# Kernel optimization log

Measured on AMD Instinct MI355X. Metric: run time of the kernel, lower is better.

The kernel has to match this reference:

```python
import jax, jax.numpy as jnp
import numpy as np

# Qwen3 MoE sparse block reference.
# E experts, top-k routing with softmax probs, normalized top-k weights,
# gated-SiLU expert MLPs (gate/up H->I, down I->H), weighted scatter-combine.
E, K, H, I = 8, 2, 2048, 768
B, S = 2, 2048


def setup_inputs() -> dict:
    key = jax.random.key(0)
    k0, k1, k2, k3, k4 = jax.random.split(key, 5)
    hidden_states = jax.random.normal(k0, (B, S, H), jnp.float32)
    w_router = jax.random.normal(k1, (H, E), jnp.float32) * (1.0 / np.sqrt(H))
    wi0 = jax.random.normal(k2, (E, H, I), jnp.float32) * 0.02  # gate proj
    wi1 = jax.random.normal(k3, (E, H, I), jnp.float32) * 0.02  # up proj
    wo = jax.random.normal(k4, (E, I, H), jnp.float32) * 0.02   # down proj
    return {"hidden_states": hidden_states, "w_router": w_router,
            "wi0": wi0, "wi1": wi1, "wo": wo}


def _moe(hidden_states, w_router, wi0, wi1, wo):
    b, s, h = hidden_states.shape
    x = hidden_states.reshape(-1, h)                       # [T, H]
    router_logits = x @ w_router                           # [T, E]
    probs = jax.nn.softmax(router_logits.astype(jnp.float32), axis=-1)
    top_w, top_i = jax.lax.top_k(probs, K)                 # [T, K]
    # norm_topk_prob = True
    top_w = top_w / jnp.sum(top_w, axis=-1, keepdims=True)
    top_w = top_w.astype(x.dtype)
    # per-(expert, token) combine weight; zero for unrouted pairs -> same math
    # as the original gather/MLP/scatter-add over selected tokens.
    onehot = jax.nn.one_hot(top_i, E, dtype=x.dtype)       # [T, K, E]
    comb = jnp.einsum('tk,tke->et', top_w, onehot)         # [E, T]
    g = jax.nn.silu(jnp.einsum('th,ehi->eti', x, wi0))     # [E, T, I]
    u = jnp.einsum('th,ehi->eti', x, wi1)                  # [E, T, I]
    y = jnp.einsum('eti,eih->eth', g * u, wo)              # [E, T, H]
    out = jnp.einsum('et,eth->th', comb, y)                # [T, H]
    return out.reshape(b, s, h), router_logits


def reference(hidden_states, w_router, wi0, wi1, wo):
    return _moe(hidden_states, w_router, wi0, wi1, wo)
```

## Files before the change

### kernel.cpp

```cpp
#include <hip/hip_runtime.h>

#define T_TOK 4096
#define H_DIM 2048
#define I_DIM 768
#define E_NUM 8

typedef __attribute__((ext_vector_type(8))) short bf16x8;
typedef __attribute__((ext_vector_type(4))) float f32x4;

__device__ __forceinline__ unsigned short f2bf(float f) {
  union { float f; unsigned int u; } c; c.f = f;
  unsigned int r = c.u + 0x7fffu + ((c.u >> 16) & 1u);
  return (unsigned short)(r >> 16);
}

__device__ __forceinline__ void gl_lds16(const unsigned short* g, unsigned short* l) {
  __builtin_amdgcn_global_load_lds(
      (const __attribute__((address_space(1))) unsigned int*)g,
      (__attribute__((address_space(3))) unsigned int*)l, 16, 0, 0);
}

__global__ __launch_bounds__(256) void transpose_cast_kernel(
    const float* __restrict__ src, unsigned short* __restrict__ dst,
    int K, int N)
{
  const int e = blockIdx.z;
  const int kb = blockIdx.y * 64, nb = blockIdx.x * 64;
  src += (size_t)e * K * N + (size_t)kb * N + nb;
  dst += (size_t)e * N * K + (size_t)nb * K + kb;
  __shared__ float tile[64][65];
  const int tid = threadIdx.x;
  const int lr = tid >> 4, lc = (tid & 15) * 4;
#pragma unroll
  for (int it = 0; it < 4; ++it) {
    float4 v = *(const float4*)(src + (size_t)(lr + it * 16) * N + lc);
    tile[lr + it * 16][lc]     = v.x;
    tile[lr + it * 16][lc + 1] = v.y;
    tile[lr + it * 16][lc + 2] = v.z;
    tile[lr + it * 16][lc + 3] = v.w;
  }
  __syncthreads();
  const int wn = tid >> 2, wk = (tid & 3) * 16;
  union { uint4 u[2]; unsigned short h[16]; } o;
#pragma unroll
  for (int j = 0; j < 16; ++j) o.h[j] = f2bf(tile[wk + j][wn]);
  *(uint4*)(dst + (size_t)wn * K + wk)     = o.u[0];
  *(uint4*)(dst + (size_t)wn * K + wk + 8) = o.u[1];
}

#define RTOK 8
__global__ __launch_bounds__(256) void router_kernel(
    const float* __restrict__ x,
    const float* __restrict__ wr,
    unsigned short* __restrict__ xbf,
    float* __restrict__ logits_out,
    int* __restrict__ counts,
    int* __restrict__ entries,
    float* __restrict__ entry_w)
{
  const int tid = threadIdx.x;
  const int w = tid >> 6, lane = tid & 63;
  const int t0 = blockIdx.x * RTOK;
  const int hb = w * 512 + lane * 8;

  float wreg[8][8];
#pragma unroll
  for (int r = 0; r < 8; ++r) {
    *(float4*)&wreg[r][0] = *(const float4*)(wr + (size_t)(hb + r) * E_NUM);
    *(float4*)&wreg[r][4] = *(const float4*)(wr + (size_t)(hb + r) * E_NUM + 4);
  }

  __shared__ float red[RTOK][4][E_NUM];
  __shared__ float lg[RTOK][E_NUM];
  __shared__ int   ch_i[RTOK][2];
  __shared__ float ch_w[RTOK][2];

  for (int tt = 0; tt < RTOK; ++tt) {
    const int t = t0 + tt;
    float xv[8];
    *(float4*)&xv[0] = *(const float4*)(x + (size_t)t * H_DIM + hb);
    *(float4*)&xv[4] = *(const float4*)(x + (size_t)t * H_DIM + hb + 4);
    union { uint4 u; unsigned short h[8]; } o;
#pragma unroll
    for (int j = 0; j < 8; ++j) o.h[j] = f2bf(xv[j]);
    *(uint4*)(xbf + (size_t)t * H_DIM + hb) = o.u;

    float acc[E_NUM];
#pragma unroll
    for (int e = 0; e < E_NUM; ++e) acc[e] = 0.f;
#pragma unroll
    for (int r = 0; r < 8; ++r)
#pragma unroll
      for (int e = 0; e < E_NUM; ++e) acc[e] = fmaf(xv[r], wreg[r][e], acc[e]);
#pragma unroll
    for (int off = 32; off > 0; off >>= 1)
#pragma unroll
      for (int e = 0; e < E_NUM; ++e) acc[e] += __shfl_down(acc[e], off);
    if (lane == 0)
#pragma unroll
      for (int e = 0; e < E_NUM; ++e) red[tt][w][e] = acc[e];
  }
  __syncthreads();

  if (tid < RTOK * E_NUM) {
    const int tt = tid >> 3, e = tid & 7;
    float l = red[tt][0][e] + red[tt][1][e] + red[tt][2][e] + red[tt][3][e];
    lg[tt][e] = l;
    logits_out[(size_t)(t0 + tt) * E_NUM + e] = l;
  }
  __syncthreads();

  if (tid < RTOK) {
    const int tt = tid;
    float m1 = lg[tt][0]; int i1 = 0;
#pragma unroll
    for (int e = 1; e < E_NUM; ++e) if (lg[tt][e] > m1) { m1 = lg[tt][e]; i1 = e; }
    float m2 = -3.4e38f; int i2 = -1;
#pragma unroll
    for (int e = 0; e < E_NUM; ++e) if (e != i1 && lg[tt][e] > m2) { m2 = lg[tt][e]; i2 = e; }
    float w1 = 1.f / (1.f + __expf(m2 - m1));
    ch_i[tt][0] = i1; ch_i[tt][1] = i2;
    ch_w[tt][0] = w1; ch_w[tt][1] = 1.f - w1;
  }
  __syncthreads();

  if (tid < E_NUM) {
    const int e = tid;
    int cnt = 0;
#pragma unroll
    for (int tt = 0; tt < RTOK; ++tt) {
      if (ch_i[tt][0] == e) ++cnt;
      if (ch_i[tt][1] == e) ++cnt;
    }
    if (cnt > 0) {
      int base = atomicAdd(&counts[e], cnt);
      int pos = 0;
#pragma unroll
      for (int tt = 0; tt < RTOK; ++tt) {
#pragma unroll
        for (int k = 0; k < 2; ++k) {
          if (ch_i[tt][k] == e) {
            entries[e * T_TOK + base + pos] = (t0 + tt) * 2 + k;
            entry_w[e * T_TOK + base + pos] = ch_w[tt][k];
            ++pos;
          }
        }
      }
    }
  }
}

#define FRAG(arr, row, cb) \
  (*(const bf16x8*)(&(arr)[((row) << 6) + ((((cb)) ^ ((row) & 7)) << 3)]))

#define MAX_MB 72

__global__ __launch_bounds__(256) void moe_up_kernel(
    const unsigned short* __restrict__ xbf,
    const unsigned short* __restrict__ wgt,
    const unsigned short* __restrict__ wut,
    const int* __restrict__ counts,
    const int* __restrict__ entries,
    unsigned short* __restrict__ act)
{
  const int bid = blockIdx.x;
  const int nb = bid % (I_DIM / 64);
  const int mbl = bid / (I_DIM / 64);
  int e = -1, m0 = 0, cnt = 0, cum = 0;
#pragma unroll
  for (int ee = 0; ee < E_NUM; ++ee) {
    int c = counts[ee];
    int nmb = (c + 127) >> 7;
    if (e < 0 && mbl < cum + nmb) { e = ee; m0 = (mbl - cum) << 7; cnt = c; }
    cum += nmb;
  }
  if (e < 0) return;
  const int n0 = nb * 64;
  const int tid = threadIdx.x;

  __shared__ __align__(16) unsigned short As[128 * 64];
  __shared__ __align__(16) unsigned short Bg[64 * 64];
  __shared__ __align__(16) unsigned short Bu[64 * 64];
  __shared__ int rowp[128];

  if (tid < 128) rowp[tid] = (m0 + tid < cnt) ? entries[e * T_TOK + m0 + tid] : -1;
  __syncthreads();

  const int w = tid >> 6, lane = tid & 63;
  const int lrow = lane >> 3, lchunk = lane & 7;
  const int jj = lchunk ^ lrow;

  const unsigned short* wg_e = wgt + (size_t)e * I_DIM * H_DIM + (size_t)n0 * H_DIM;
  const unsigned short* wu_e = wut + (size_t)e * I_DIM * H_DIM + (size_t)n0 * H_DIM;
  const unsigned short* gA[4];
  unsigned short* lA[4];
#pragma unroll
  for (int t4 = 0; t4 < 4; ++t4) {
    int r = (t4 * 4 + w) * 8 + lrow;
    int p = rowp[r];
    int tok = (p >= 0) ? (p >> 1) : 0;
    gA[t4] = xbf + (size_t)tok * H_DIM + jj * 8;
    lA[t4] = As + (t4 * 4 + w) * 512;
  }
  const unsigned short* gG[2]; const unsigned short* gU[2]; unsigned short* lG[2]; unsigned short* lU[2];
#pragma unroll
  for (int t2 = 0; t2 < 2; ++t2) {
    int r = (t2 * 4 + w) * 8 + lrow;
    gG[t2] = wg_e + (size_t)r * H_DIM + jj * 8;
    gU[t2] = wu_e + (size_t)r * H_DIM + jj * 8;
    lG[t2] = Bg + (t2 * 4 + w) * 512;
    lU[t2] = Bu + (t2 * 4 + w) * 512;
  }

  f32x4 accg[4][2], accu[4][2];
#pragma unroll
  for (int i = 0; i < 4; ++i)
#pragma unroll
    for (int j = 0; j < 2; ++j) {
      accg[i][j] = (f32x4){0.f, 0.f, 0.f, 0.f};
      accu[i][j] = (f32x4){0.f, 0.f, 0.f, 0.f};
    }

  const int msub = (w >> 1) * 64, nsub = (w & 1) * 32;
  const int fm = lane & 15, fq = lane >> 4;

  for (int kt = 0; kt < H_DIM; kt += 64) {
#pragma unroll
    for (int t4 = 0; t4 < 4; ++t4) gl_lds16(gA[t4] + kt, lA[t4]);
#pragma unroll
    for (int t2 = 0; t2 < 2; ++t2) {
      gl_lds16(gG[t2] + kt, lG[t2]);
      gl_lds16(gU[t2] + kt, lU[t2]);
    }
    __syncthreads();
#pragma unroll
    for (int ks = 0; ks < 64; ks += 32) {
      const int cb = (ks >> 3) + fq;
      bf16x8 a[4], bg[2], bu[2];
#pragma unroll
      for (int mi = 0; mi < 4; ++mi)
        a[mi] = FRAG(As, msub + mi * 16 + fm, cb);
#pragma unroll
      for (int ni = 0; ni < 2; ++ni) {
        bg[ni] = FRAG(Bg, nsub + ni * 16 + fm, cb);
        bu[ni] = FRAG(Bu, nsub + ni * 16 + fm, cb);
      }
#pragma unroll
      for (int mi = 0; mi < 4; ++mi)
#pragma unroll
        for (int ni = 0; ni < 2; ++ni) {
          accg[mi][ni] = __builtin_amdgcn_mfma_f32_16x16x32_bf16(a[mi], bg[ni], accg[mi][ni], 0, 0, 0);
          accu[mi][ni] = __builtin_amdgcn_mfma_f32_16x16x32_bf16(a[mi], bu[ni], accu[mi][ni], 0, 0, 0);
        }
    }
    __syncthreads();
  }
#pragma unroll
  for (int mi = 0; mi < 4; ++mi) {
#pragma unroll
    for (int r = 0; r < 4; ++r) {
      int ml = msub + mi * 16 + fq * 4 + r;
      int p = rowp[ml];
      if (p < 0) continue;
      size_t base = (size_t)p * I_DIM + n0 + nsub + fm;
#pragma unroll
      for (int ni = 0; ni < 2; ++ni) {
        float g = accg[mi][ni][r];
        float u = accu[mi][ni][r];
        float h = g / (1.f + __expf(-g)) * u;
        act[base + ni * 16] = f2bf(h);
      }
    }
  }
}

__global__ __launch_bounds__(256) void moe_down_kernel(
    const unsigned short* __restrict__ act,
    const unsigned short* __restrict__ wot,
    const int* __restrict__ counts,
    const int* __restrict__ entries,
    const float* __restrict__ entry_w,
    float* __restrict__ out)
{
  const int bid = blockIdx.x;
  const int nb = bid % (H_DIM / 128);
  const int mbl = bid / (H_DIM / 128);
  int e = -1, m0 = 0, cnt = 0, cum = 0;
#pragma unroll
  for (int ee = 0; ee < E_NUM; ++ee) {
    int c = counts[ee];
    int nmb = (c + 127) >> 7;
    if (e < 0 && mbl < cum + nmb) { e = ee; m0 = (mbl - cum) << 7; cnt = c; }
    cum += nmb;
  }
  if (e < 0) return;
  const int n0 = nb * 128;
  const int tid = threadIdx.x;

  __shared__ __align__(16) unsigned short As[128 * 64];
  __shared__ __align__(16) unsigned short Bt[128 * 64];
  __shared__ int rowp[128];
  __shared__ float roww[128];

  if (tid < 128) {
    int idx = m0 + tid;
    rowp[tid] = (idx < cnt) ? entries[e * T_TOK + idx] : -1;
    roww[tid] = (idx < cnt) ? entry_w[e * T_TOK + idx] : 0.f;
  }
  __syncthreads();

  const int w = tid >> 6, lane = tid & 63;
  const int lrow = lane >> 3, lchunk = lane & 7;
  const int jj = lchunk ^ lrow;

  const unsigned short* wo_e = wot + (size_t)e * H_DIM * I_DIM + (size_t)n0 * I_DIM;
  const unsigned short* gA[4]; unsigned short* lA[4];
  const unsigned short* gB[4]; unsigned short* lB[4];
#pragma unroll
  for (int t4 = 0; t4 < 4; ++t4) {
    int r = (t4 * 4 + w) * 8 + lrow;
    int p = rowp[r];
    int pr = (p >= 0) ? p : 0;
    gA[t4] = act + (size_t)pr * I_DIM + jj * 8;
    lA[t4] = As + (t4 * 4 + w) * 512;
    gB[t4] = wo_e + (size_t)r * I_DIM + jj * 8;
    lB[t4] = Bt + (t4 * 4 + w) * 512;
  }

  f32x4 acc[4][4];
#pragma unroll
  for (int i = 0; i < 4; ++i)
#pragma unroll
    for (int j = 0; j < 4; ++j) acc[i][j] = (f32x4){0.f, 0.f, 0.f, 0.f};

  const int msub = (w >> 1) * 64, nsub = (w & 1) * 64;
  const int fm = lane & 15, fq = lane >> 4;

  for (int kt = 0; kt < I_DIM; kt += 64) {
#pragma unroll
    for (int t4 = 0; t4 < 4; ++t4) {
      gl_lds16(gA[t4] + kt, lA[t4]);
      gl_lds16(gB[t4] + kt, lB[t4]);
    }
    __syncthreads();
#pragma unroll
    for (int ks = 0; ks < 64; ks += 32) {
      const int cb = (ks >> 3) + fq;
      bf16x8 a[4], b[4];
#pragma unroll
      for (int mi = 0; mi < 4; ++mi)
        a[mi] = FRAG(As, msub + mi * 16 + fm, cb);
#pragma unroll
      for (int ni = 0; ni < 4; ++ni)
        b[ni] = FRAG(Bt, nsub + ni * 16 + fm, cb);
#pragma unroll
      for (int mi = 0; mi < 4; ++mi)
#pragma unroll
        for (int ni = 0; ni < 4; ++ni)
          acc[mi][ni] = __builtin_amdgcn_mfma_f32_16x16x32_bf16(a[mi], b[ni], acc[mi][ni], 0, 0, 0);
    }
    __syncthreads();
  }
#pragma unroll
  for (int mi = 0; mi < 4; ++mi) {
#pragma unroll
    for (int r = 0; r < 4; ++r) {
      int ml = msub + mi * 16 + fq * 4 + r;
      int p = rowp[ml];
      if (p < 0) continue;
      float wt = roww[ml];
      float* dst = out + (size_t)(p >> 1) * H_DIM + n0 + nsub + fm;
#pragma unroll
      for (int ni = 0; ni < 4; ++ni)
        atomicAdd(dst + ni * 16, acc[mi][ni][r] * wt);
    }
  }
}

extern "C" void kernel_launch(void* const* d_in, const int* in_sizes, int n_in,
                              void* d_out, int out_size, void* d_ws, size_t ws_size,
                              hipStream_t stream) {
  const float* x   = (const float*)d_in[0];
  const float* wr  = (const float*)d_in[1];
  const float* wi0 = (const float*)d_in[2];
  const float* wi1 = (const float*)d_in[3];
  const float* wo  = (const float*)d_in[4];
  float* out = (float*)d_out;
  float* logits_out = out + (size_t)T_TOK * H_DIM;

  char* w = (char*)d_ws;
  int* counts    = (int*)w;
  int* entries   = (int*)(w + 64);
  float* entry_w = (float*)(w + 64 + (size_t)E_NUM * T_TOK * 4);
  size_t off = 64 + 2 * (size_t)E_NUM * T_TOK * 4;
  unsigned short* xbf = (unsigned short*)(w + off); off += (size_t)T_TOK * H_DIM * 2;
  unsigned short* wgt = (unsigned short*)(w + off); off += (size_t)E_NUM * H_DIM * I_DIM * 2;
  unsigned short* wut = (unsigned short*)(w + off); off += (size_t)E_NUM * H_DIM * I_DIM * 2;
  unsigned short* wot = (unsigned short*)(w + off); off += (size_t)E_NUM * H_DIM * I_DIM * 2;
  unsigned short* act = (unsigned short*)(w + off);

  hipMemsetAsync(d_out, 0, (size_t)T_TOK * H_DIM * sizeof(float), stream);
  hipMemsetAsync(counts, 0, 64, stream);
  transpose_cast_kernel<<<dim3(I_DIM / 64, H_DIM / 64, E_NUM), 256, 0, stream>>>(
      wi0, wgt, H_DIM, I_DIM);
  transpose_cast_kernel<<<dim3(I_DIM / 64, H_DIM / 64, E_NUM), 256, 0, stream>>>(
      wi1, wut, H_DIM, I_DIM);
  transpose_cast_kernel<<<dim3(H_DIM / 64, I_DIM / 64, E_NUM), 256, 0, stream>>>(
      wo, wot, I_DIM, H_DIM);
  router_kernel<<<T_TOK / RTOK, 256, 0, stream>>>(x, wr, xbf, logits_out, counts, entries, entry_w);
  moe_up_kernel<<<dim3(MAX_MB * (I_DIM / 64)), 256, 0, stream>>>(
      xbf, wgt, wut, counts, entries, act);
  moe_down_kernel<<<dim3(MAX_MB * (H_DIM / 128)), 256, 0, stream>>>(
      act, wot, counts, entries, entry_w, out);
}
```

Measured before the change: 417.3 us.

## Double-buffer LDS tiles in both expert GEMMs with async prefetch two stages ahead

Both grouped GEMM kernels (gate/up and down) now keep two LDS buffers per operand. The next K tile is loaded via global_load_lds while the current tile is being computed, using raw barriers and vmcnt waits instead of __syncthreads. This hides global-load latency behind MFMA work. MFMA sections are also raised in wave priority with s_setprio. LDS use per block doubles, which may reduce occupancy. The hand-written waitcnt values must match the number of loads issued per stage.

```diff
diff --git a/kernel.cpp b/kernel.cpp
--- a/kernel.cpp
+++ b/kernel.cpp
@@ -19,6 +19,14 @@
       (const __attribute__((address_space(1))) unsigned int*)g,
       (__attribute__((address_space(3))) unsigned int*)l, 16, 0, 0);
 }
+
+__device__ __forceinline__ void barrier_raw() {
+  asm volatile("" ::: "memory");
+  __builtin_amdgcn_s_barrier();
+  asm volatile("" ::: "memory");
+}
+#define VM_WAIT8 asm volatile("s_waitcnt vmcnt(8)" ::: "memory")
+#define VM_WAIT0 asm volatile("s_waitcnt vmcnt(0)" ::: "memory")
 
 __global__ __launch_bounds__(256) void transpose_cast_kernel(
     const float* __restrict__ src, unsigned short* __restrict__ dst,
@@ -178,9 +186,9 @@
   const int n0 = nb * 64;
   const int tid = threadIdx.x;
 
-  __shared__ __align__(16) unsigned short As[128 * 64];
-  __shared__ __align__(16) unsigned short Bg[64 * 64];
-  __shared__ __align__(16) unsigned short Bu[64 * 64];
+  __shared__ __align__(16) unsigned short As[2][128 * 64];
+  __shared__ __align__(16) unsigned short Bg[2][64 * 64];
+  __shared__ __align__(16) unsigned short Bu[2][64 * 64];
   __shared__ int rowp[128];
 
   if (tid < 128) rowp[tid] = (m0 + tid < cnt) ? entries[e * T_TOK + m0 + tid] : -1;
@@ -193,23 +201,23 @@
   const unsigned short* wg_e = wgt + (size_t)e * I_DIM * H_DIM + (size_t)n0 * H_DIM;
   const unsigned short* wu_e = wut + (size_t)e * I_DIM * H_DIM + (size_t)n0 * H_DIM;
   const unsigned short* gA[4];
-  unsigned short* lA[4];
+  int aoff[4];
 #pragma unroll
   for (int t4 = 0; t4 < 4; ++t4) {
     int r = (t4 * 4 + w) * 8 + lrow;
     int p = rowp[r];
     int tok = (p >= 0) ? (p >> 1) : 0;
     gA[t4] = xbf + (size_t)tok * H_DIM + jj * 8;
-    lA[t4] = As + (t4 * 4 + w) * 512;
-  }
-  const unsigned short* gG[2]; const unsigned short* gU[2]; unsigned short* lG[2]; unsigned short* lU[2];
+    aoff[t4] = (t4 * 4 + w) * 512;
+  }
+  const unsigned short* gG[2]; const unsigned short* gU[2];
+  int boff[2];
 #pragma unroll
   for (int t2 = 0; t2 < 2; ++t2) {
     int r = (t2 * 4 + w) * 8 + lrow;
     gG[t2] = wg_e + (size_t)r * H_DIM + jj * 8;
     gU[t2] = wu_e + (size_t)r * H_DIM + jj * 8;
-    lG[t2] = Bg + (t2 * 4 + w) * 512;
-    lU[t2] = Bu + (t2 * 4 + w) * 512;
+    boff[t2] = (t2 * 4 + w) * 512;
   }
 
   f32x4 accg[4][2], accu[4][2];
@@ -224,27 +232,40 @@
   const int msub = (w >> 1) * 64, nsub = (w & 1) * 32;
   const int fm = lane & 15, fq = lane >> 4;
 
-  for (int kt = 0; kt < H_DIM; kt += 64) {
-#pragma unroll
-    for (int t4 = 0; t4 < 4; ++t4) gl_lds16(gA[t4] + kt, lA[t4]);
+  auto stage = [&](int kt, int b) {
+#pragma unroll
+    for (int t4 = 0; t4 < 4; ++t4) gl_lds16(gA[t4] + kt, &As[b][aoff[t4]]);
 #pragma unroll
     for (int t2 = 0; t2 < 2; ++t2) {
-      gl_lds16(gG[t2] + kt, lG[t2]);
-      gl_lds16(gU[t2] + kt, lU[t2]);
-    }
-    __syncthreads();
+      gl_lds16(gG[t2] + kt, &Bg[b][boff[t2]]);
+      gl_lds16(gU[t2] + kt, &Bu[b][boff[t2]]);
+    }
+  };
+
+  stage(0, 0);
+  stage(64, 1);
+  VM_WAIT8;
+  barrier_raw();
+
+  int cur = 0;
+  const int NT = H_DIM / 64;
+  for (int t = 0; t < NT; ++t) {
+    const unsigned short* Ac  = As[cur];
+    const unsigned short* Bgc = Bg[cur];
+    const unsigned short* Buc = Bu[cur];
 #pragma unroll
     for (int ks = 0; ks < 64; ks += 32) {
       const int cb = (ks >> 3) + fq;
       bf16x8 a[4], bg[2], bu[2];
 #pragma unroll
       for (int mi = 0; mi < 4; ++mi)
-        a[mi] = FRAG(As, msub + mi * 16 + fm, cb);
+        a[mi] = FRAG(Ac, msub + mi * 16 + fm, cb);
 #pragma unroll
       for (int ni = 0; ni < 2; ++ni) {
-        bg[ni] = FRAG(Bg, nsub + ni * 16 + fm, cb);
-        bu[ni] = FRAG(Bu, nsub + ni * 16 + fm, cb);
+        bg[ni] = FRAG(Bgc, nsub + ni * 16 + fm, cb);
+        bu[ni] = FRAG(Buc, nsub + ni * 16 + fm, cb);
       }
+      __builtin_amdgcn_s_setprio(1);
 #pragma unroll
       for (int mi = 0; mi < 4; ++mi)
 #pragma unroll
@@ -252,9 +273,19 @@
           accg[mi][ni] = __builtin_amdgcn_mfma_f32_16x16x32_bf16(a[mi], bg[ni], accg[mi][ni], 0, 0, 0);
           accu[mi][ni] = __builtin_amdgcn_mfma_f32_16x16x32_bf16(a[mi], bu[ni], accu[mi][ni], 0, 0, 0);
         }
-    }
-    __syncthreads();
-  }
+      __builtin_amdgcn_s_setprio(0);
+    }
+    barrier_raw();
+    if (t + 2 < NT) {
+      stage((t + 2) * 64, cur);
+      VM_WAIT8;
+    } else {
+      VM_WAIT0;
+    }
+    barrier_raw();
+    cur ^= 1;
+  }
+
 #pragma unroll
   for (int mi = 0; mi < 4; ++mi) {
 #pragma unroll
@@ -297,8 +328,8 @@
   const int n0 = nb * 128;
   const int tid = threadIdx.x;
 
-  __shared__ __align__(16) unsigned short As[128 * 64];
-  __shared__ __align__(16) unsigned short Bt[128 * 64];
+  __shared__ __align__(16) unsigned short As[2][128 * 64];
+  __shared__ __align__(16) unsigned short Bt[2][128 * 64];
   __shared__ int rowp[128];
   __shared__ float roww[128];
 
@@ -314,17 +345,16 @@
   const int jj = lchunk ^ lrow;
 
   const unsigned short* wo_e = wot + (size_t)e * H_DIM * I_DIM + (size_t)n0 * I_DIM;
-  const unsigned short* gA[4]; unsigned short* lA[4];
-  const unsigned short* gB[4]; unsigned short* lB[4];
+  const unsigned short* gA[4]; const unsigned short* gB[4];
+  int coff[4];
 #pragma unroll
   for (int t4 = 0; t4 < 4; ++t4) {
     int r = (t4 * 4 + w) * 8 + lrow;
     int p = rowp[r];
     int pr = (p >= 0) ? p : 0;
     gA[t4] = act + (size_t)pr * I_DIM + jj * 8;
-    lA[t4] = As + (t4 * 4 + w) * 512;
     gB[t4] = wo_e + (size_t)r * I_DIM + jj * 8;
-    lB[t4] = Bt + (t4 * 4 + w) * 512;
+    coff[t4] = (t4 * 4 + w) * 512;
   }
 
   f32x4 acc[4][4];
@@ -336,31 +366,53 @@
   const int msub = (w >> 1) * 64, nsub = (w & 1) * 64;
   const int fm = lane & 15, fq = lane >> 4;
 
-  for (int kt = 0; kt < I_DIM; kt += 64) {
+  auto stage = [&](int kt, int b) {
 #pragma unroll
     for (int t4 = 0; t4 < 4; ++t4) {
-      gl_lds16(gA[t4] + kt, lA[t4]);
-      gl_lds16(gB[t4] + kt, lB[t4]);
-    }
-    __syncthreads();
+      gl_lds16(gA[t4] + kt, &As[b][coff[t4]]);
+      gl_lds16(gB[t4] + kt, &Bt[b][coff[t4]]);
+    }
+  };
+
+  stage(0, 0);
+  stage(64, 1);
+  VM_WAIT8;
+  barrier_raw();
+
+  int cur = 0;
+  const int NT = I_DIM / 64;
+  for (int t = 0; t < NT; ++t) {
+    const unsigned short* Ac = As[cur];
+    const unsigned short* Bc = Bt[cur];
 #pragma unroll
     for (int ks = 0; ks < 64; ks += 32) {
       const int cb = (ks >> 3) + fq;
       bf16x8 a[4], b[4];
 #pragma unroll
       for (int mi = 0; mi < 4; ++mi)
-        a[mi] = FRAG(As, msub + mi * 16 + fm, cb);
+        a[mi] = FRAG(Ac, msub + mi * 16 + fm, cb);
 #pragma unroll
       for (int ni = 0; ni < 4; ++ni)
-        b[ni] = FRAG(Bt, nsub + ni * 16 + fm, cb);
+        b[ni] = FRAG(Bc, nsub + ni * 16 + fm, cb);
+      __builtin_amdgcn_s_setprio(1);
 #pragma unroll
       for (int mi = 0; mi < 4; ++mi)
 #pragma unroll
         for (int ni = 0; ni < 4; ++ni)
           acc[mi][ni] = __builtin_amdgcn_mfma_f32_16x16x32_bf16(a[mi], b[ni], acc[mi][ni], 0, 0, 0);
-    }
-    __syncthreads();
-  }
+      __builtin_amdgcn_s_setprio(0);
+    }
+    barrier_raw();
+    if (t + 2 < NT) {
+      stage((t + 2) * 64, cur);
+      VM_WAIT8;
+    } else {
+      VM_WAIT0;
+    }
+    barrier_raw();
+    cur ^= 1;
+  }
+
 #pragma unroll
   for (int mi = 0; mi < 4; ++mi) {
 #pragma unroll
```

New measurement: 410.9 us. Within noise of the previous version (-1.5%).

## Merge weight transpose-casts and router into one prep kernel; swizzle GEMM block order

Applied to the files above, without the earlier changes.

Combines the three weight transpose/cast launches and the router launch into a single prep kernel that dispatches on block index, using a shared-memory buffer reused across the roles. This removes three launch boundaries and lets the router blocks run alongside the transpose blocks. The up and down GEMM kernels also remap blockIdx so consecutive blocks stride across the grid in eight groups, which likely spreads work across XCDs or balances them. The remap assumes the grid size divides by 8 and is meant to help cache locality and load balance.

```diff
diff --git a/kernel.cpp b/kernel.cpp
--- a/kernel.cpp
+++ b/kernel.cpp
@@ -20,47 +20,67 @@
       (__attribute__((address_space(3))) unsigned int*)l, 16, 0, 0);
 }
 
-__global__ __launch_bounds__(256) void transpose_cast_kernel(
-    const float* __restrict__ src, unsigned short* __restrict__ dst,
-    int K, int N)
-{
-  const int e = blockIdx.z;
-  const int kb = blockIdx.y * 64, nb = blockIdx.x * 64;
-  src += (size_t)e * K * N + (size_t)kb * N + nb;
-  dst += (size_t)e * N * K + (size_t)nb * K + kb;
-  __shared__ float tile[64][65];
-  const int tid = threadIdx.x;
-  const int lr = tid >> 4, lc = (tid & 15) * 4;
-#pragma unroll
-  for (int it = 0; it < 4; ++it) {
-    float4 v = *(const float4*)(src + (size_t)(lr + it * 16) * N + lc);
-    tile[lr + it * 16][lc]     = v.x;
-    tile[lr + it * 16][lc + 1] = v.y;
-    tile[lr + it * 16][lc + 2] = v.z;
-    tile[lr + it * 16][lc + 3] = v.w;
-  }
-  __syncthreads();
-  const int wn = tid >> 2, wk = (tid & 3) * 16;
-  union { uint4 u[2]; unsigned short h[16]; } o;
-#pragma unroll
-  for (int j = 0; j < 16; ++j) o.h[j] = f2bf(tile[wk + j][wn]);
-  *(uint4*)(dst + (size_t)wn * K + wk)     = o.u[0];
-  *(uint4*)(dst + (size_t)wn * K + wk + 8) = o.u[1];
-}
-
 #define RTOK 8
-__global__ __launch_bounds__(256) void router_kernel(
-    const float* __restrict__ x,
-    const float* __restrict__ wr,
-    unsigned short* __restrict__ xbf,
-    float* __restrict__ logits_out,
-    int* __restrict__ counts,
-    int* __restrict__ entries,
+#define PREP_T0 3072
+#define PREP_T1 6144
+#define PREP_T2 9216
+#define PREP_TOTAL (PREP_T2 + T_TOK / RTOK)
+
+struct RouterSmem {
+  float red[RTOK][4][E_NUM];
+  float lg[RTOK][E_NUM];
+  int   ch_i[RTOK][2];
+  float ch_w[RTOK][2];
+};
+
+__global__ __launch_bounds__(256) void prep_kernel(
+    const float* __restrict__ wi0, const float* __restrict__ wi1,
+    const float* __restrict__ wo,
+    unsigned short* __restrict__ wgt, unsigned short* __restrict__ wut,
+    unsigned short* __restrict__ wot,
+    const float* __restrict__ x, const float* __restrict__ wr,
+    unsigned short* __restrict__ xbf, float* __restrict__ logits_out,
+    int* __restrict__ counts, int* __restrict__ entries,
     float* __restrict__ entry_w)
 {
+  __shared__ __align__(16) char smem[64 * 65 * 4];
+  const int bid = blockIdx.x;
   const int tid = threadIdx.x;
+
+  if (bid < PREP_T2) {
+    const float* src; unsigned short* dst; int K, N, lb;
+    if (bid < PREP_T0)      { src = wi0; dst = wgt; K = H_DIM; N = I_DIM; lb = bid; }
+    else if (bid < PREP_T1) { src = wi1; dst = wut; K = H_DIM; N = I_DIM; lb = bid - PREP_T0; }
+    else                    { src = wo;  dst = wot; K = I_DIM; N = H_DIM; lb = bid - PREP_T1; }
+    const int nx = N / 64, ky = K / 64;
+    const int nb = (lb % nx) * 64;
+    const int kb = ((lb / nx) % ky) * 64;
+    const int e  = lb / (nx * ky);
+    src += (size_t)e * K * N + (size_t)kb * N + nb;
+    dst += (size_t)e * N * K + (size_t)nb * K + kb;
+    float (*tile)[65] = (float(*)[65])smem;
+    const int lr = tid >> 4, lc = (tid & 15) * 4;
+#pragma unroll
+    for (int it = 0; it < 4; ++it) {
+      float4 v = *(const float4*)(src + (size_t)(lr + it * 16) * N + lc);
+      tile[lr + it * 16][lc]     = v.x;
+      tile[lr + it * 16][lc + 1] = v.y;
+      tile[lr + it * 16][lc + 2] = v.z;
+      tile[lr + it * 16][lc + 3] = v.w;
+    }
+    __syncthreads();
+    const int wn = tid >> 2, wk = (tid & 3) * 16;
+    union { uint4 u[2]; unsigned short h[16]; } o;
+#pragma unroll
+    for (int j = 0; j < 16; ++j) o.h[j] = f2bf(tile[wk + j][wn]);
+    *(uint4*)(dst + (size_t)wn * K + wk)     = o.u[0];
+    *(uint4*)(dst + (size_t)wn * K + wk + 8) = o.u[1];
+    return;
+  }
+
+  RouterSmem* rs = (RouterSmem*)smem;
   const int w = tid >> 6, lane = tid & 63;
-  const int t0 = blockIdx.x * RTOK;
+  const int t0 = (bid - PREP_T2) * RTOK;
   const int hb = w * 512 + lane * 8;
 
   float wreg[8][8];
@@ -69,11 +89,6 @@
     *(float4*)&wreg[r][0] = *(const float4*)(wr + (size_t)(hb + r) * E_NUM);
     *(float4*)&wreg[r][4] = *(const float4*)(wr + (size_t)(hb + r) * E_NUM + 4);
   }
-
-  __shared__ float red[RTOK][4][E_NUM];
-  __shared__ float lg[RTOK][E_NUM];
-  __shared__ int   ch_i[RTOK][2];
-  __shared__ float ch_w[RTOK][2];
 
   for (int tt = 0; tt < RTOK; ++tt) {
     const int t = t0 + tt;
@@ -98,29 +113,29 @@
       for (int e = 0; e < E_NUM; ++e) acc[e] += __shfl_down(acc[e], off);
     if (lane == 0)
 #pragma unroll
-      for (int e = 0; e < E_NUM; ++e) red[tt][w][e] = acc[e];
+      for (int e = 0; e < E_NUM; ++e) rs->red[tt][w][e] = acc[e];
   }
   __syncthreads();
 
   if (tid < RTOK * E_NUM) {
     const int tt = tid >> 3, e = tid & 7;
-    float l = red[tt][0][e] + red[tt][1][e] + red[tt][2][e] + red[tt][3][e];
-    lg[tt][e] = l;
+    float l = rs->red[tt][0][e] + rs->red[tt][1][e] + rs->red[tt][2][e] + rs->red[tt][3][e];
+    rs->lg[tt][e] = l;
     logits_out[(size_t)(t0 + tt) * E_NUM + e] = l;
   }
   __syncthreads();
 
   if (tid < RTOK) {
     const int tt = tid;
-    float m1 = lg[tt][0]; int i1 = 0;
-#pragma unroll
-    for (int e = 1; e < E_NUM; ++e) if (lg[tt][e] > m1) { m1 = lg[tt][e]; i1 = e; }
+    float m1 = rs->lg[tt][0]; int i1 = 0;
+#pragma unroll
+    for (int e = 1; e < E_NUM; ++e) if (rs->lg[tt][e] > m1) { m1 = rs->lg[tt][e]; i1 = e; }
     float m2 = -3.4e38f; int i2 = -1;
 #pragma unroll
-    for (int e = 0; e < E_NUM; ++e) if (e != i1 && lg[tt][e] > m2) { m2 = lg[tt][e]; i2 = e; }
+    for (int e = 0; e < E_NUM; ++e) if (e != i1 && rs->lg[tt][e] > m2) { m2 = rs->lg[tt][e]; i2 = e; }
     float w1 = 1.f / (1.f + __expf(m2 - m1));
-    ch_i[tt][0] = i1; ch_i[tt][1] = i2;
-    ch_w[tt][0] = w1; ch_w[tt][1] = 1.f - w1;
+    rs->ch_i[tt][0] = i1; rs->ch_i[tt][1] = i2;
+    rs->ch_w[tt][0] = w1; rs->ch_w[tt][1] = 1.f - w1;
   }
   __syncthreads();
 
@@ -129,8 +144,8 @@
     int cnt = 0;
 #pragma unroll
     for (int tt = 0; tt < RTOK; ++tt) {
-      if (ch_i[tt][0] == e) ++cnt;
-      if (ch_i[tt][1] == e) ++cnt;
+      if (rs->ch_i[tt][0] == e) ++cnt;
+      if (rs->ch_i[tt][1] == e) ++cnt;
     }
     if (cnt > 0) {
       int base = atomicAdd(&counts[e], cnt);
@@ -139,9 +154,9 @@
       for (int tt = 0; tt < RTOK; ++tt) {
 #pragma unroll
         for (int k = 0; k < 2; ++k) {
-          if (ch_i[tt][k] == e) {
+          if (rs->ch_i[tt][k] == e) {
             entries[e * T_TOK + base + pos] = (t0 + tt) * 2 + k;
-            entry_w[e * T_TOK + base + pos] = ch_w[tt][k];
+            entry_w[e * T_TOK + base + pos] = rs->ch_w[tt][k];
             ++pos;
           }
         }
@@ -154,6 +169,8 @@
   (*(const bf16x8*)(&(arr)[((row) << 6) + ((((cb)) ^ ((row) & 7)) << 3)]))
 
 #define MAX_MB 72
+#define UP_NB (I_DIM / 64)
+#define DN_NB (H_DIM / 128)
 
 __global__ __launch_bounds__(256) void moe_up_kernel(
     const unsigned short* __restrict__ xbf,
@@ -163,9 +180,9 @@
     const int* __restrict__ entries,
     unsigned short* __restrict__ act)
 {
-  const int bid = blockIdx.x;
-  const int nb = bid % (I_DIM / 64);
-  const int mbl = bid / (I_DIM / 64);
+  const int sb = (blockIdx.x & 7) * (MAX_MB * UP_NB / 8) + (blockIdx.x >> 3);
+  const int nb = sb % UP_NB;
+  const int mbl = sb / UP_NB;
   int e = -1, m0 = 0, cnt = 0, cum = 0;
 #pragma unroll
   for (int ee = 0; ee < E_NUM; ++ee) {
@@ -282,9 +299,9 @@
     const float* __restrict__ entry_w,
     float* __restrict__ out)
 {
-  const int bid = blockIdx.x;
-  const int nb = bid % (H_DIM / 128);
-  const int mbl = bid / (H_DIM / 128);
+  const int sb = (blockIdx.x & 7) * (MAX_MB * DN_NB / 8) + (blockIdx.x >> 3);
+  const int nb = sb % DN_NB;
+  const int mbl = sb / DN_NB;
   int e = -1, m0 = 0, cnt = 0, cum = 0;
 #pragma unroll
   for (int ee = 0; ee < E_NUM; ++ee) {
@@ -401,15 +418,10 @@
 
   hipMemsetAsync(d_out, 0, (size_t)T_TOK * H_DIM * sizeof(float), stream);
   hipMemsetAsync(counts, 0, 64, stream);
-  transpose_cast_kernel<<<dim3(I_DIM / 64, H_DIM / 64, E_NUM), 256, 0, stream>>>(
-      wi0, wgt, H_DIM, I_DIM);
-  transpose_cast_kernel<<<dim3(I_DIM / 64, H_DIM / 64, E_NUM), 256, 0, stream>>>(
-      wi1, wut, H_DIM, I_DIM);
-  transpose_cast_kernel<<<dim3(H_DIM / 64, I_DIM / 64, E_NUM), 256, 0, stream>>>(
-      wo, wot, I_DIM, H_DIM);
-  router_kernel<<<T_TOK / RTOK, 256, 0, stream>>>(x, wr, xbf, logits_out, counts, entries, entry_w);
-  moe_up_kernel<<<dim3(MAX_MB * (I_DIM / 64)), 256, 0, stream>>>(
+  prep_kernel<<<dim3(PREP_TOTAL), 256, 0, stream>>>(
+      wi0, wi1, wo, wgt, wut, wot, x, wr, xbf, logits_out, counts, entries, entry_w);
+  moe_up_kernel<<<dim3(MAX_MB * UP_NB), 256, 0, stream>>>(
       xbf, wgt, wut, counts, entries, act);
-  moe_down_kernel<<<dim3(MAX_MB * (H_DIM / 128)), 256, 0, stream>>>(
+  moe_down_kernel<<<dim3(MAX_MB * DN_NB), 256, 0, stream>>>(
       act, wot, counts, entries, entry_w, out);
 }
```

Result: no change. 410.4 us (-1.6%).
